# Kernel tuning notes

Measured on AMD Instinct MI355X. Metric: run time of the kernel, lower is better.

Reference implementation:

```python
import jax, jax.numpy as jnp
import numpy as np

B, N, M = 256, 4096, 16384
NUM_STEPS = 50
DT = 1.0
FP_THRES = 1e-3


def setup_inputs() -> dict:
    key = jax.random.key(0)
    k1, k2 = jax.random.split(key)
    inp = jax.random.normal(k1, (B, N, 1), dtype=jnp.float32)
    # xavier_normal for W [hidden, input]: std = sqrt(2/(fan_in+fan_out))
    std = np.sqrt(2.0 / (M + N)).astype(np.float32)
    W = jax.random.normal(k2, (M, N), dtype=jnp.float32) * std
    beta = jnp.float32(1.0)
    tau = jnp.float32(1.0)
    return {"input": inp, "W": W, "beta": beta, "tau": tau}


def reference(input, W, beta, tau):
    # Hopfield fixed-point iteration: v <- v + dt/tau * (W^T softmax(beta W v) - v)
    # input_mode='init' => state starts at input, no external current, no clamping.
    state0 = input  # [B, N, 1]
    done0 = jnp.array(False)

    def step(carry, _):
        state, done = carry
        h = jnp.einsum('mn,bno->bmo', W, state)            # [B, M, 1]
        f = jax.nn.softmax(beta * h, axis=-2)              # softmax over memory dim
        v_inst = jnp.einsum('mn,bmo->bno', W, f)           # [B, N, 1]
        new = state + (DT / tau) * (v_inst - state)
        # torch: update_magnitude = (prev_state - state).norm() (global Frobenius norm)
        upd = jnp.linalg.norm((new - state).reshape(-1))
        state_out = jnp.where(done, state, new)            # freeze once converged
        done = done | (upd <= FP_THRES)
        return (state_out, done), None

    (state, _), _ = jax.lax.scan(step, (state0, done0), None, length=NUM_STEPS)
    return state
```

## Files before the change

kernel.cpp:

```cpp
#include <hip/hip_runtime.h>

typedef __attribute__((ext_vector_type(8))) short short8;
typedef __attribute__((ext_vector_type(4))) float f32x4;
typedef __attribute__((ext_vector_type(2))) unsigned int u32x2;
typedef __attribute__((ext_vector_type(4))) unsigned int u32x4;

#define WS_ET   0u
#define WS_P2   8388608u
#define WS_ST   41943040u
#define WS_SB   46137344u
#define WS_CS   48234496u
#define WS_UG   48285696u
#define WS_CNT  48285952u
#define WS_WB   48298752u
#define WS_WBT  182516480u
#define WS_END  316734208u

#define WO_ET  0u
#define WO_P2  8388608u
#define WO_ST  25165824u
#define WO_SB  29360128u
#define WO_CS  31457280u
#define WO_UG  31508480u
#define WO_CNT 31508736u
#define WO_END 31534336u

static __device__ __forceinline__ unsigned short f2bf(float x) {
  union { float f; unsigned u; } v; v.f = x;
  unsigned r = v.u + 0x7FFFu + ((v.u >> 16) & 1u);
  return (unsigned short)(r >> 16);
}

static __device__ __forceinline__ void gl_lds16(const void* g, void* l) {
  __builtin_amdgcn_global_load_lds(
      (const __attribute__((address_space(1))) void*)g,
      (__attribute__((address_space(3))) void*)l, 16, 0, 0);
}

static __device__ __forceinline__ bool conv_before(const float* uG, int s) {
  bool d = false;
  for (int i = 0; i < s; ++i) d |= (uG[i] <= (-1.0f + 1.0e-6f));
  return d;
}

__global__ void sentinel_kernel(float* out, float v) { out[0] = v; }

__global__ void __launch_bounds__(256)
k0_setup(const float* __restrict__ inp, float* __restrict__ St,
         unsigned short* __restrict__ Sb, float* __restrict__ csG,
         float* __restrict__ uG, int* __restrict__ cnt)
{
  const int t = threadIdx.x, blk = blockIdx.x;
  if (blk == 0) {
    for (int i = t; i < 50 * 256; i += 256) csG[i] = 0.0f;
    if (t < 64) uG[t] = -1.0f;
  } else if (blk == 1) {
    for (int i = t; i < 50 * 128; i += 256) cnt[i] = 0;
  }
  #pragma unroll
  for (int i = 0; i < 8; ++i) {
    int idx = blk * 2048 + i * 256 + t;
    float v = inp[idx];
    Sb[idx] = f2bf(v);
    St[(idx & 4095) * 256 + (idx >> 12)] = v;
  }
}

__global__ void __launch_bounds__(256)
k0w_conv(const float* __restrict__ Wg, unsigned short* __restrict__ Wb,
         unsigned short* __restrict__ WbT)
{
  __shared__ unsigned short Tl[64][66];
  const int t = threadIdx.x;
  const int r = t >> 2, q = t & 3;
  for (int i = 0; i < 4; ++i) {
    const int ti = blockIdx.x * 4 + i;
    const int m0 = (ti >> 6) * 64;
    const int n0 = (ti & 63) * 64;
    const float* src = Wg + (size_t)(m0 + r) * 4096 + n0 + q * 16;
    unsigned short h[16] __attribute__((aligned(16)));
    #pragma unroll
    for (int v = 0; v < 4; ++v) {
      float4 f = *(const float4*)(src + v * 4);
      h[v*4+0] = f2bf(f.x); h[v*4+1] = f2bf(f.y);
      h[v*4+2] = f2bf(f.z); h[v*4+3] = f2bf(f.w);
    }
    unsigned short* wbp = Wb + (size_t)(m0 + r) * 4096 + n0 + q * 16;
    *(u32x4*)wbp       = *(const u32x4*)h;
    *(u32x4*)(wbp + 8) = *(const u32x4*)(h + 8);
    if (i) __syncthreads();
    #pragma unroll
    for (int k = 0; k < 16; ++k) Tl[r][q * 16 + k] = h[k];
    __syncthreads();
    unsigned short g[16] __attribute__((aligned(16)));
    const int nn = t >> 2;
    #pragma unroll
    for (int k = 0; k < 16; ++k) g[k] = Tl[q * 16 + k][nn];
    unsigned short* wtp = WbT + (size_t)(n0 + nn) * 16384 + m0 + q * 16;
    *(u32x4*)wtp       = *(const u32x4*)g;
    *(u32x4*)(wtp + 8) = *(const u32x4*)(g + 8);
  }
}

template<int ITERS>
static __device__ __forceinline__ void gemm_core(
    const unsigned short* __restrict__ Ag, const size_t lda, const int arow0,
    const unsigned short* __restrict__ Bg, const size_t ldb, const int brow0,
    const int kbase, unsigned short* smem, f32x4 (&acc)[4][4], const int t)
{
  const int lane = t & 63, wv = t >> 6;
  const int l15 = lane & 15, quad = lane >> 4;
  const int wr = wv >> 1, wc = wv & 1;
  const int xr = l15 & 7;
  unsigned short* As0 = smem;
  unsigned short* As1 = smem + 8192;
  unsigned short* Bs0 = smem + 16384;
  unsigned short* Bs1 = smem + 24576;
  const int srow = wv * 8 + (lane >> 3);
  const int ks   = ((lane & 7) ^ (lane >> 3)) * 8;
  const unsigned short* gA = Ag + (size_t)(arow0 + srow) * lda + kbase + ks;
  const unsigned short* gB = Bg + (size_t)(brow0 + srow) * ldb + kbase + ks;
  const int sb = wv * 512;

#define STAGE(itv, Ad, Bd)                                                        \
  { _Pragma("unroll") for (int j_ = 0; j_ < 4; ++j_) {                            \
      gl_lds16(gA + (size_t)j_ * 32 * lda + (size_t)(itv) * 64, (Ad) + j_ * 2048 + sb); \
      gl_lds16(gB + (size_t)j_ * 32 * ldb + (size_t)(itv) * 64, (Bd) + j_ * 2048 + sb); } }

  STAGE(0, As0, Bs0);
  __syncthreads();
  #pragma unroll 2
  for (int it = 0; it < ITERS; ++it) {
    unsigned short *Asc, *Bsc, *Asn, *Bsn;
    if (it & 1) { Asc = As1; Bsc = Bs1; Asn = As0; Bsn = Bs0; }
    else        { Asc = As0; Bsc = Bs0; Asn = As1; Bsn = Bs1; }
    if (it + 1 < ITERS) STAGE(it + 1, Asn, Bsn);
    #pragma unroll
    for (int kk = 0; kk < 2; ++kk) {
      short8 af[4], bq[4];
      const int so = ((kk * 4 + quad) ^ xr) << 3;
      #pragma unroll
      for (int r = 0; r < 4; ++r)
        af[r] = *(const short8*)(Asc + (wr * 64 + r * 16 + l15) * 64 + so);
      #pragma unroll
      for (int c = 0; c < 4; ++c)
        bq[c] = *(const short8*)(Bsc + (wc * 64 + c * 16 + l15) * 64 + so);
      #pragma unroll
      for (int r = 0; r < 4; ++r)
        #pragma unroll
        for (int c = 0; c < 4; ++c)
          acc[r][c] = __builtin_amdgcn_mfma_f32_16x16x32_bf16(af[r], bq[c], acc[r][c], 0, 0, 0);
    }
    __syncthreads();
  }
#undef STAGE
}

__global__ void __launch_bounds__(256, 2)
k1_gemm1(const unsigned short* __restrict__ Wb, const float* __restrict__ betap,
         const unsigned short* __restrict__ Sb, unsigned short* __restrict__ Et,
         float* __restrict__ csG, const float* __restrict__ uG, int s)
{
  if (conv_before(uG, s)) return;
  __shared__ __align__(16) unsigned char smem_[65536];
  const int t = threadIdx.x;
  const int w = ((blockIdx.x & 7) << 5) | (blockIdx.x >> 3);
  const int mt = w >> 1, bt = w & 1;
  const int m0 = mt * 128, b0 = bt * 128;

  f32x4 acc[4][4];
  #pragma unroll
  for (int r = 0; r < 4; ++r)
    #pragma unroll
    for (int c = 0; c < 4; ++c) { f32x4 z = {0.f,0.f,0.f,0.f}; acc[r][c] = z; }

  gemm_core<64>(Wb, 4096, m0, Sb, 4096, b0, 0, (unsigned short*)smem_, acc, t);

  const float beta = betap[0];
  const int lane = t & 63, wv = t >> 6, l15 = lane & 15, quad = lane >> 4;
  const int wr = wv >> 1, wc = wv & 1;
  #pragma unroll
  for (int c = 0; c < 4; ++c) {
    const int b = b0 + wc * 64 + c * 16 + l15;
    float cs = 0.0f;
    #pragma unroll
    for (int r = 0; r < 4; ++r) {
      unsigned short eb[4] __attribute__((aligned(8)));
      #pragma unroll
      for (int j = 0; j < 4; ++j) {
        float e = __expf(beta * acc[r][c][j]);
        cs += e;
        eb[j] = f2bf(e);
      }
      *(u32x2*)(Et + (size_t)b * 16384 + m0 + wr * 64 + r * 16 + quad * 4) = *(const u32x2*)eb;
    }
    cs += __shfl_xor(cs, 16, 64);
    cs += __shfl_xor(cs, 32, 64);
    if (quad == 0) atomicAdd(&csG[s * 256 + b], cs);
  }
}

__global__ void __launch_bounds__(256, 2)
k2_gemm2(const unsigned short* __restrict__ WbT, const float* __restrict__ taup,
         const unsigned short* __restrict__ Et, float* __restrict__ P2,
         float* __restrict__ St, unsigned short* __restrict__ Sb,
         const float* __restrict__ csG, float* __restrict__ uG,
         int* __restrict__ cnt, float* __restrict__ out, int s)
{
  if (conv_before(uG, s)) return;
  __shared__ __align__(16) unsigned char smem_[65536];
  const int t = threadIdx.x;
  const int w = ((blockIdx.x & 7) << 6) | (blockIdx.x >> 3);
  const int kc = w >> 6, nt = (w & 63) >> 1, bt = w & 1;
  const int n0 = nt * 128, b0 = bt * 128;

  f32x4 acc[4][4];
  #pragma unroll
  for (int r = 0; r < 4; ++r)
    #pragma unroll
    for (int c = 0; c < 4; ++c) { f32x4 z = {0.f,0.f,0.f,0.f}; acc[r][c] = z; }

  gemm_core<32>(WbT, 16384, n0, Et, 16384, b0, kc * 2048, (unsigned short*)smem_, acc, t);

  const int lane = t & 63, wv = t >> 6, l15 = lane & 15, quad = lane >> 4;
  const int wr = wv >> 1, wc = wv & 1;
  float* Pd = P2 + (size_t)kc * 1048576;
  #pragma unroll
  for (int r = 0; r < 4; ++r) {
    const int n = n0 + wr * 64 + r * 16 + quad * 4;
    #pragma unroll
    for (int c = 0; c < 4; ++c) {
      const int b = b0 + wc * 64 + c * 16 + l15;
      #pragma unroll
      for (int j = 0; j < 4; ++j)
        Pd[(size_t)(n + j) * 256 + b] = acc[r][c][j];
    }
  }

  __syncthreads();
  if (t == 0) {
    __threadfence();
    int old = atomicAdd(&cnt[s * 64 + (nt * 2 + bt)], 1);
    *(volatile int*)smem_ = (old == 7) ? 1 : 0;
  }
  __syncthreads();
  const bool last = (*(volatile int*)smem_ != 0);
  if (!last) return;
  __threadfence();
  __syncthreads();

  const float dtau = 1.0f / taup[0];
  float* T = (float*)smem_;
  float d2 = 0.0f;
  {
    const int bl = t & 127, th = t >> 7;
    const int bg = b0 + bl;
    const float inv = 1.0f / csG[s * 256 + bg];
    for (int i = 0; i < 64; ++i) {
      const int nl = i * 2 + th;
      const int n = n0 + nl;
      const float* pp = P2 + (size_t)n * 256 + bg;
      float sum = ((pp[0]       + pp[1048576]) + (pp[2097152] + pp[3145728]))
                + ((pp[4194304] + pp[5242880]) + (pp[6291456] + pp[7340032]));
      float v = sum * inv;
      float old = St[n * 256 + bg];
      float nw = old + dtau * (v - old);
      float d = nw - old;
      d2 += d * d;
      St[n * 256 + bg] = nw;
      T[bl * 128 + (nl ^ (bl & 31))] = nw;
    }
  }
  __syncthreads();
  {
    const int nl = t & 127, th = t >> 7;
    #pragma unroll 4
    for (int p = 0; p < 64; ++p) {
      const int bl = p * 2 + th;
      out[(size_t)(b0 + bl) * 4096 + n0 + nl] = T[bl * 128 + (nl ^ (bl & 31))];
    }
  }
  {
    const int np = (t & 63) * 2, th = t >> 6;
    #pragma unroll 4
    for (int p = 0; p < 32; ++p) {
      const int bl = p * 4 + th;
      const int sw = bl & 31;
      float x0 = T[bl * 128 + (np ^ sw)];
      float x1 = T[bl * 128 + ((np + 1) ^ sw)];
      unsigned u = (unsigned)f2bf(x0) | ((unsigned)f2bf(x1) << 16);
      *(unsigned*)(Sb + (size_t)(b0 + bl) * 4096 + n0 + np) = u;
    }
  }
  #pragma unroll
  for (int o = 32; o > 0; o >>= 1) d2 += __shfl_down(d2, o, 64);
  __syncthreads();
  float* red = (float*)smem_;
  if (lane == 0) red[wv] = d2;
  __syncthreads();
  if (t == 0) atomicAdd(&uG[s], red[0] + red[1] + red[2] + red[3]);
}

__global__ void __launch_bounds__(256, 2)
k1_gemm1_o(const float* __restrict__ Wg, const float* __restrict__ betap,
           const unsigned short* __restrict__ Sb, unsigned short* __restrict__ Et,
           float* __restrict__ csG, const float* __restrict__ uG, int s)
{
  if (conv_before(uG, s)) return;
  __shared__ __align__(16) unsigned char smem[36864];
  const int t = threadIdx.x;
  const int lane = t & 63;
  const int wv = t >> 6;
  const int quad = lane >> 4;
  const int l15 = lane & 15;
  const float beta = betap[0];

  const int m0 = blockIdx.x * 32;
  unsigned short* As0 = (unsigned short*)(smem);
  unsigned short* As1 = (unsigned short*)(smem + 2048);
  unsigned short* Bs0 = (unsigned short*)(smem + 4096);
  unsigned short* Bs1 = (unsigned short*)(smem + 20480);
  const int ar = t >> 3;
  const int ac = (t & 7) * 4;
  const float* gA = Wg + (size_t)(m0 + ar) * 4096 + ac;
  const int brow = wv * 16 + (lane >> 2);
  const int bcol = (lane & 3) * 8;

  f32x4 acc[2][4];
  #pragma unroll
  for (int r = 0; r < 2; ++r)
    #pragma unroll
    for (int c = 0; c < 4; ++c) { f32x4 z = {0.f,0.f,0.f,0.f}; acc[r][c] = z; }

  float4 arA, arB;
#define LOADA1(itv, dst) { dst = *(const float4*)(gA + (itv) * 32); }
#define WRITEA1(Ad, src) { unsigned short p_[4] __attribute__((aligned(8)));        \
      p_[0]=f2bf((src).x); p_[1]=f2bf((src).y); p_[2]=f2bf((src).z); p_[3]=f2bf((src).w); \
      *(u32x2*)((Ad) + ar * 32 + ac) = *(const u32x2*)p_; }
#define STAGEB1(itv, Bd) { const int k0_ = (itv) * 32 + bcol;                       \
      _Pragma("unroll") for (int j_ = 0; j_ < 4; ++j_)                              \
        gl_lds16(Sb + (size_t)(j_ * 64 + brow) * 4096 + k0_, (Bd) + j_ * 2048 + wv * 512); }

  LOADA1(0, arA); STAGEB1(0, Bs0); WRITEA1(As0, arA); LOADA1(1, arB);
  __syncthreads();

  #pragma unroll 2
  for (int it = 0; it < 128; ++it) {
    unsigned short *Asc, *Bsc, *Asn, *Bsn;
    float4 *arC, *arN;
    if (it & 1) { Asc = As1; Bsc = Bs1; Asn = As0; Bsn = Bs0; arC = &arA; arN = &arB; }
    else        { Asc = As0; Bsc = Bs0; Asn = As1; Bsn = Bs1; arC = &arB; arN = &arA; }
    if (it + 2 < 128) LOADA1(it + 2, (*arN));
    if (it + 1 < 128) { STAGEB1(it + 1, Bsn); WRITEA1(Asn, (*arC)); }
    short8 af[2], bq[4];
    #pragma unroll
    for (int r = 0; r < 2; ++r) af[r] = *(const short8*)(Asc + (16 * r + l15) * 32 + quad * 8);
    #pragma unroll
    for (int c = 0; c < 4; ++c) bq[c] = *(const short8*)(Bsc + (64 * wv + 16 * c + l15) * 32 + quad * 8);
    #pragma unroll
    for (int r = 0; r < 2; ++r)
      #pragma unroll
      for (int c = 0; c < 4; ++c)
        acc[r][c] = __builtin_amdgcn_mfma_f32_16x16x32_bf16(af[r], bq[c], acc[r][c], 0, 0, 0);
    __syncthreads();
  }
#undef LOADA1
#undef WRITEA1
#undef STAGEB1
  #pragma unroll
  for (int c = 0; c < 4; ++c) {
    const int b = 64 * wv + 16 * c + l15;
    float cs = 0.0f;
    #pragma unroll
    for (int r = 0; r < 2; ++r) {
      unsigned short eb[4] __attribute__((aligned(8)));
      #pragma unroll
      for (int j = 0; j < 4; ++j) {
        float e = __expf(beta * acc[r][c][j]);
        cs += e;
        eb[j] = f2bf(e);
      }
      *(u32x2*)(Et + (size_t)b * 16384 + m0 + 16 * r + quad * 4) = *(const u32x2*)eb;
    }
    cs += __shfl_xor(cs, 16, 64);
    cs += __shfl_xor(cs, 32, 64);
    if (quad == 0) atomicAdd(&csG[s * 256 + b], cs);
  }
}

__global__ void __launch_bounds__(256, 2)
k2_gemm2_o(const float* __restrict__ Wg, const float* __restrict__ taup,
           const unsigned short* __restrict__ Et, float* __restrict__ P2,
           float* __restrict__ St, unsigned short* __restrict__ Sb,
           const float* __restrict__ csG, float* __restrict__ uG,
           int* __restrict__ cnt, float* __restrict__ out, int s)
{
  if (conv_before(uG, s)) return;
  __shared__ __align__(16) unsigned char smem[37888];
  __shared__ int lastF;
  const int t = threadIdx.x;
  const int lane = t & 63;
  const int wv = t >> 6;
  const int quad = lane >> 4;
  const int l15 = lane & 15;
  const int rt = blockIdx.x & 127;
  const int kc = blockIdx.x >> 7;
  const int n0 = rt * 32;
  const int mb = kc * 4096;

  unsigned short* As0 = (unsigned short*)(smem);
  unsigned short* As1 = (unsigned short*)(smem + 2560);
  unsigned short* Bs0 = (unsigned short*)(smem + 5120);
  unsigned short* Bs1 = (unsigned short*)(smem + 21504);
  const int mp = (t >> 4) * 2;
  const int ng = (t & 15) * 2;
  const int brow = wv * 16 + (lane >> 2);
  const int bcol = (lane & 3) * 8;

  f32x4 acc[2][4];
  #pragma unroll
  for (int r = 0; r < 2; ++r)
    #pragma unroll
    for (int c = 0; c < 4; ++c) { f32x4 z = {0.f,0.f,0.f,0.f}; acc[r][c] = z; }

  float2 aA0, aA1, aB0, aB1;
#define LOADA2(itv, d0, d1) { const float* g_ = Wg + (size_t)(mb + (itv) * 32 + mp) * 4096 + n0 + ng; \
      d0 = *(const float2*)g_; d1 = *(const float2*)(g_ + 4096); }
#define WRITEA2(Ad, d0, d1) {                                                       \
      unsigned x0_ = (unsigned)f2bf((d0).x) | ((unsigned)f2bf((d1).x) << 16);       \
      unsigned x1_ = (unsigned)f2bf((d0).y) | ((unsigned)f2bf((d1).y) << 16);       \
      *(unsigned*)((Ad) + ng * 40 + mp) = x0_;                                      \
      *(unsigned*)((Ad) + (ng + 1) * 40 + mp) = x1_; }
#define STAGEB2(itv, Bd) { const int k0_ = mb + (itv) * 32 + bcol;                  \
      _Pragma("unroll") for (int j_ = 0; j_ < 4; ++j_)                              \
        gl_lds16(Et + (size_t)(j_ * 64 + brow) * 16384 + k0_, (Bd) + j_ * 2048 + wv * 512); }

  LOADA2(0, aA0, aA1); STAGEB2(0, Bs0); WRITEA2(As0, aA0, aA1); LOADA2(1, aB0, aB1);
  __syncthreads();

  #pragma unroll 2
  for (int it = 0; it < 128; ++it) {
    unsigned short *Asc, *Bsc, *Asn, *Bsn;
    float2 *c0, *c1, *n0p, *n1p;
    if (it & 1) { Asc = As1; Bsc = Bs1; Asn = As0; Bsn = Bs0; c0 = &aA0; c1 = &aA1; n0p = &aB0; n1p = &aB1; }
    else        { Asc = As0; Bsc = Bs0; Asn = As1; Bsn = Bs1; c0 = &aB0; c1 = &aB1; n0p = &aA0; n1p = &aA1; }
    if (it + 2 < 128) LOADA2(it + 2, (*n0p), (*n1p));
    if (it + 1 < 128) { STAGEB2(it + 1, Bsn); WRITEA2(Asn, (*c0), (*c1)); }
    short8 af[2], bq[4];
    #pragma unroll
    for (int r = 0; r < 2; ++r) af[r] = *(const short8*)(Asc + (16 * r + l15) * 40 + quad * 8);
    #pragma unroll
    for (int c = 0; c < 4; ++c) bq[c] = *(const short8*)(Bsc + (64 * wv + 16 * c + l15) * 32 + quad * 8);
    #pragma unroll
    for (int r = 0; r < 2; ++r)
      #pragma unroll
      for (int c = 0; c < 4; ++c)
        acc[r][c] = __builtin_amdgcn_mfma_f32_16x16x32_bf16(af[r], bq[c], acc[r][c], 0, 0, 0);
    __syncthreads();
  }
#undef LOADA2
#undef WRITEA2
#undef STAGEB2
  float* Pd = P2 + (size_t)kc * 1048576;
  #pragma unroll
  for (int r = 0; r < 2; ++r)
    #pragma unroll
    for (int c = 0; c < 4; ++c) {
      const int b = 64 * wv + 16 * c + l15;
      #pragma unroll
      for (int j = 0; j < 4; ++j)
        Pd[(size_t)(n0 + 16 * r + quad * 4 + j) * 256 + b] = acc[r][c][j];
    }

  __syncthreads();
  if (t == 0) {
    __threadfence();
    int old = atomicAdd(&cnt[s * 128 + rt], 1);
    lastF = (old == 3);
  }
  __syncthreads();
  if (!lastF) return;
  __threadfence();

  const float dtau = 1.0f / taup[0];
  const float inv = 1.0f / csG[s * 256 + t];
  float* T = (float*)smem;
  float d2 = 0.0f;
  for (int i = 0; i < 32; ++i) {
    const int n = n0 + i;
    const float* pp = P2 + (size_t)n * 256 + t;
    float sum = pp[0] + pp[1048576] + pp[2097152] + pp[3145728];
    float v = sum * inv;
    float old = St[n * 256 + t];
    float nw = old + dtau * (v - old);
    float d = nw - old;
    d2 += d * d;
    St[n * 256 + t] = nw;
    T[t * 33 + i] = nw;
  }
  __syncthreads();
  #pragma unroll 4
  for (int p = 0; p < 32; ++p) {
    const int b = p * 8 + (t >> 5);
    const int nl = t & 31;
    out[(size_t)b * 4096 + n0 + nl] = T[b * 33 + nl];
  }
  #pragma unroll 4
  for (int p = 0; p < 16; ++p) {
    const int b = p * 16 + (t >> 4);
    const int np = (t & 15) * 2;
    unsigned u = (unsigned)f2bf(T[b * 33 + np]) | ((unsigned)f2bf(T[b * 33 + np + 1]) << 16);
    *(unsigned*)(Sb + (size_t)b * 4096 + n0 + np) = u;
  }
  #pragma unroll
  for (int o = 32; o > 0; o >>= 1) d2 += __shfl_down(d2, o, 64);
  __syncthreads();
  float* red = (float*)smem;
  if (lane == 0) red[wv] = d2;
  __syncthreads();
  if (t == 0) atomicAdd(&uG[s], red[0] + red[1] + red[2] + red[3]);
}

extern "C" void kernel_launch(void* const* d_in, const int* in_sizes, int n_in,
                              void* d_out, int out_size, void* d_ws, size_t ws_size,
                              hipStream_t stream) {
  const float* inp   = (const float*)d_in[0];
  const float* W     = (const float*)d_in[1];
  const float* betap = (const float*)d_in[2];
  const float* taup  = (const float*)d_in[3];
  float* out = (float*)d_out;
  char* ws = (char*)d_ws;

  if (ws_size >= (size_t)WS_END) {
    unsigned short* Et = (unsigned short*)(ws + WS_ET);
    float*          P2 = (float*)(ws + WS_P2);
    float*          St = (float*)(ws + WS_ST);
    unsigned short* Sb = (unsigned short*)(ws + WS_SB);
    float*          cs = (float*)(ws + WS_CS);
    float*          uG = (float*)(ws + WS_UG);
    int*            cn = (int*)(ws + WS_CNT);
    unsigned short* Wb = (unsigned short*)(ws + WS_WB);
    unsigned short* Wt = (unsigned short*)(ws + WS_WBT);

    hipLaunchKernelGGL(k0_setup, dim3(512), dim3(256), 0, stream, inp, St, Sb, cs, uG, cn);
    hipLaunchKernelGGL(k0w_conv, dim3(4096), dim3(256), 0, stream, W, Wb, Wt);
    for (int s = 0; s < 50; ++s) {
      hipLaunchKernelGGL(k1_gemm1, dim3(256), dim3(256), 0, stream, Wb, betap, Sb, Et, cs, uG, s);
      hipLaunchKernelGGL(k2_gemm2, dim3(512), dim3(256), 0, stream, Wt, taup, Et, P2, St, Sb, cs, uG, cn, out, s);
    }
  } else if (ws_size >= (size_t)WO_END) {
    unsigned short* Et = (unsigned short*)(ws + WO_ET);
    float*          P2 = (float*)(ws + WO_P2);
    float*          St = (float*)(ws + WO_ST);
    unsigned short* Sb = (unsigned short*)(ws + WO_SB);
    float*          cs = (float*)(ws + WO_CS);
    float*          uG = (float*)(ws + WO_UG);
    int*            cn = (int*)(ws + WO_CNT);

    hipLaunchKernelGGL(k0_setup, dim3(512), dim3(256), 0, stream, inp, St, Sb, cs, uG, cn);
    for (int s = 0; s < 50; ++s) {
      hipLaunchKernelGGL(k1_gemm1_o, dim3(512), dim3(256), 0, stream, W, betap, Sb, Et, cs, uG, s);
      hipLaunchKernelGGL(k2_gemm2_o, dim3(512), dim3(256), 0, stream, W, taup, Et, P2, St, Sb, cs, uG, cn, out, s);
    }
  } else {
    hipLaunchKernelGGL(sentinel_kernel, dim3(1), dim3(1), 0, stream, out, 1.0e6f);
  }
}
```

Measured before the change: 1.178 ms.

## Fuse all Hopfield iterations into one persistent cooperative kernel with grid syncs

```diff
diff --git a/kernel.cpp b/kernel.cpp
--- a/kernel.cpp
+++ b/kernel.cpp
@@ -1,4 +1,7 @@
 #include <hip/hip_runtime.h>
+#include <hip/hip_cooperative_groups.h>
+
+namespace cg = cooperative_groups;
 
 typedef __attribute__((ext_vector_type(8))) short short8;
 typedef __attribute__((ext_vector_type(4))) float f32x4;
@@ -102,12 +105,13 @@
   }
 }
 
-template<int ITERS>
+template<int ITERS, int BROWS>
 static __device__ __forceinline__ void gemm_core(
     const unsigned short* __restrict__ Ag, const size_t lda, const int arow0,
     const unsigned short* __restrict__ Bg, const size_t ldb, const int brow0,
-    const int kbase, unsigned short* smem, f32x4 (&acc)[4][4], const int t)
+    const int kbase, unsigned short* smem, f32x4 (&acc)[4][BROWS / 32], const int t)
 {
+  constexpr int NC = BROWS / 32;
   const int lane = t & 63, wv = t >> 6;
   const int l15 = lane & 15, quad = lane >> 4;
   const int wr = wv >> 1, wc = wv & 1;
@@ -115,45 +119,168 @@
   unsigned short* As0 = smem;
   unsigned short* As1 = smem + 8192;
   unsigned short* Bs0 = smem + 16384;
-  unsigned short* Bs1 = smem + 24576;
+  unsigned short* Bs1 = Bs0 + BROWS * 64;
   const int srow = wv * 8 + (lane >> 3);
   const int ks   = ((lane & 7) ^ (lane >> 3)) * 8;
   const unsigned short* gA = Ag + (size_t)(arow0 + srow) * lda + kbase + ks;
   const unsigned short* gB = Bg + (size_t)(brow0 + srow) * ldb + kbase + ks;
   const int sb = wv * 512;
 
-#define STAGE(itv, Ad, Bd)                                                        \
-  { _Pragma("unroll") for (int j_ = 0; j_ < 4; ++j_) {                            \
+#define STAGE_(itv, Ad, Bd)                                                       \
+  { _Pragma("unroll") for (int j_ = 0; j_ < 4; ++j_)                              \
       gl_lds16(gA + (size_t)j_ * 32 * lda + (size_t)(itv) * 64, (Ad) + j_ * 2048 + sb); \
-      gl_lds16(gB + (size_t)j_ * 32 * ldb + (size_t)(itv) * 64, (Bd) + j_ * 2048 + sb); } }
-
-  STAGE(0, As0, Bs0);
+    _Pragma("unroll") for (int j_ = 0; j_ < NC; ++j_)                             \
+      gl_lds16(gB + (size_t)j_ * 32 * ldb + (size_t)(itv) * 64, (Bd) + j_ * 2048 + sb); }
+
+  STAGE_(0, As0, Bs0);
   __syncthreads();
   #pragma unroll 2
   for (int it = 0; it < ITERS; ++it) {
     unsigned short *Asc, *Bsc, *Asn, *Bsn;
     if (it & 1) { Asc = As1; Bsc = Bs1; Asn = As0; Bsn = Bs0; }
     else        { Asc = As0; Bsc = Bs0; Asn = As1; Bsn = Bs1; }
-    if (it + 1 < ITERS) STAGE(it + 1, Asn, Bsn);
+    if (it + 1 < ITERS) STAGE_(it + 1, Asn, Bsn);
     #pragma unroll
     for (int kk = 0; kk < 2; ++kk) {
-      short8 af[4], bq[4];
+      short8 af[4], bq[NC];
       const int so = ((kk * 4 + quad) ^ xr) << 3;
       #pragma unroll
       for (int r = 0; r < 4; ++r)
         af[r] = *(const short8*)(Asc + (wr * 64 + r * 16 + l15) * 64 + so);
       #pragma unroll
-      for (int c = 0; c < 4; ++c)
-        bq[c] = *(const short8*)(Bsc + (wc * 64 + c * 16 + l15) * 64 + so);
+      for (int c = 0; c < NC; ++c)
+        bq[c] = *(const short8*)(Bsc + (wc * (BROWS / 2) + c * 16 + l15) * 64 + so);
       #pragma unroll
       for (int r = 0; r < 4; ++r)
         #pragma unroll
-        for (int c = 0; c < 4; ++c)
+        for (int c = 0; c < NC; ++c)
           acc[r][c] = __builtin_amdgcn_mfma_f32_16x16x32_bf16(af[r], bq[c], acc[r][c], 0, 0, 0);
     }
     __syncthreads();
   }
-#undef STAGE
+#undef STAGE_
+}
+
+__global__ void __launch_bounds__(256, 2)
+khop_coop(const unsigned short* __restrict__ Wb, const unsigned short* __restrict__ WbT,
+          const float* __restrict__ betap, const float* __restrict__ taup,
+          unsigned short* __restrict__ Et, float* __restrict__ P2,
+          float* __restrict__ St, unsigned short* __restrict__ Sb,
+          float* __restrict__ csG, float* __restrict__ uG, float* __restrict__ out)
+{
+  cg::grid_group grid = cg::this_grid();
+  __shared__ __align__(16) unsigned char smem_[65536];
+  const int t = threadIdx.x;
+  const int blk = blockIdx.x;
+  const int w = ((blk & 7) << 6) | (blk >> 3);
+  const int lane = t & 63, wv = t >> 6;
+  const int l15 = lane & 15, quad = lane >> 4;
+  const int wr = wv >> 1, wc = wv & 1;
+  const float dtau = 1.0f / taup[0];
+  const float beta = betap[0];
+
+  for (int s = 0; s < 50; ++s) {
+    {
+      const int mt = w >> 2, bt = w & 3;
+      const int m0 = mt * 128, b0 = bt * 64;
+      f32x4 acc[4][2];
+      #pragma unroll
+      for (int r = 0; r < 4; ++r)
+        #pragma unroll
+        for (int c = 0; c < 2; ++c) { f32x4 z = {0.f,0.f,0.f,0.f}; acc[r][c] = z; }
+      gemm_core<64, 64>(Wb, 4096, m0, Sb, 4096, b0, 0, (unsigned short*)smem_, acc, t);
+      #pragma unroll
+      for (int c = 0; c < 2; ++c) {
+        const int b = b0 + wc * 32 + c * 16 + l15;
+        float cs = 0.0f;
+        #pragma unroll
+        for (int r = 0; r < 4; ++r) {
+          unsigned short eb[4] __attribute__((aligned(8)));
+          #pragma unroll
+          for (int j = 0; j < 4; ++j) {
+            float e = __expf(beta * acc[r][c][j]);
+            cs += e;
+            eb[j] = f2bf(e);
+          }
+          *(u32x2*)(Et + (size_t)b * 16384 + m0 + wr * 64 + r * 16 + quad * 4) = *(const u32x2*)eb;
+        }
+        cs += __shfl_xor(cs, 16, 64);
+        cs += __shfl_xor(cs, 32, 64);
+        if (quad == 0) atomicAdd(&csG[s * 256 + b], cs);
+      }
+    }
+    __threadfence();
+    grid.sync();
+
+    {
+      const int kc = w >> 6, nt = (w & 63) >> 1, bt2 = w & 1;
+      const int n0 = nt * 128, b0 = bt2 * 128;
+      f32x4 acc[4][4];
+      #pragma unroll
+      for (int r = 0; r < 4; ++r)
+        #pragma unroll
+        for (int c = 0; c < 4; ++c) { f32x4 z = {0.f,0.f,0.f,0.f}; acc[r][c] = z; }
+      gemm_core<32, 128>(WbT, 16384, n0, Et, 16384, b0, kc * 2048, (unsigned short*)smem_, acc, t);
+      float* Pd = P2 + (size_t)kc * 1048576;
+      #pragma unroll
+      for (int r = 0; r < 4; ++r) {
+        const int n = n0 + wr * 64 + r * 16 + quad * 4;
+        #pragma unroll
+        for (int c = 0; c < 4; ++c) {
+          const int b = b0 + wc * 64 + c * 16 + l15;
+          #pragma unroll
+          for (int j = 0; j < 4; ++j)
+            Pd[(size_t)(n + j) * 256 + b] = acc[r][c][j];
+        }
+      }
+    }
+    __threadfence();
+    grid.sync();
+
+    {
+      const int n0 = blk * 8;
+      const float inv = 1.0f / csG[s * 256 + t];
+      float* T = (float*)smem_;
+      float d2 = 0.0f;
+      #pragma unroll
+      for (int i = 0; i < 8; ++i) {
+        const int n = n0 + i;
+        const float* pp = P2 + (size_t)n * 256 + t;
+        float sum = ((pp[0]       + pp[1048576]) + (pp[2097152] + pp[3145728]))
+                  + ((pp[4194304] + pp[5242880]) + (pp[6291456] + pp[7340032]));
+        float v = sum * inv;
+        float old = St[n * 256 + t];
+        float nw = old + dtau * (v - old);
+        float d = nw - old;
+        d2 += d * d;
+        St[n * 256 + t] = nw;
+        T[t * 9 + i] = nw;
+      }
+      __syncthreads();
+      #pragma unroll
+      for (int p = 0; p < 8; ++p) {
+        const int b = p * 32 + (t >> 3);
+        out[(size_t)b * 4096 + n0 + (t & 7)] = T[b * 9 + (t & 7)];
+      }
+      #pragma unroll
+      for (int p = 0; p < 4; ++p) {
+        const int b = p * 64 + (t >> 2);
+        const int np = (t & 3) * 2;
+        unsigned u = (unsigned)f2bf(T[b * 9 + np]) | ((unsigned)f2bf(T[b * 9 + np + 1]) << 16);
+        *(unsigned*)(Sb + (size_t)b * 4096 + n0 + np) = u;
+      }
+      #pragma unroll
+      for (int o = 32; o > 0; o >>= 1) d2 += __shfl_down(d2, o, 64);
+      float* red = (float*)(smem_ + 32768);
+      if (lane == 0) red[wv] = d2;
+      __syncthreads();
+      if (t == 0) atomicAdd(&uG[s], red[0] + red[1] + red[2] + red[3]);
+    }
+    __threadfence();
+    grid.sync();
+    const float u = __hip_atomic_load(&uG[s], __ATOMIC_RELAXED, __HIP_MEMORY_SCOPE_AGENT);
+    if (u <= (-1.0f + 1.0e-6f)) break;
+  }
 }
 
 __global__ void __launch_bounds__(256, 2)
@@ -174,7 +301,7 @@
     #pragma unroll
     for (int c = 0; c < 4; ++c) { f32x4 z = {0.f,0.f,0.f,0.f}; acc[r][c] = z; }
 
-  gemm_core<64>(Wb, 4096, m0, Sb, 4096, b0, 0, (unsigned short*)smem_, acc, t);
+  gemm_core<64, 128>(Wb, 4096, m0, Sb, 4096, b0, 0, (unsigned short*)smem_, acc, t);
 
   const float beta = betap[0];
   const int lane = t & 63, wv = t >> 6, l15 = lane & 15, quad = lane >> 4;
@@ -220,7 +347,7 @@
     #pragma unroll
     for (int c = 0; c < 4; ++c) { f32x4 z = {0.f,0.f,0.f,0.f}; acc[r][c] = z; }
 
-  gemm_core<32>(WbT, 16384, n0, Et, 16384, b0, kc * 2048, (unsigned short*)smem_, acc, t);
+  gemm_core<32, 128>(WbT, 16384, n0, Et, 16384, b0, kc * 2048, (unsigned short*)smem_, acc, t);
 
   const int lane = t & 63, wv = t >> 6, l15 = lane & 15, quad = lane >> 4;
   const int wr = wv >> 1, wc = wv & 1;
@@ -544,9 +671,15 @@
 
     hipLaunchKernelGGL(k0_setup, dim3(512), dim3(256), 0, stream, inp, St, Sb, cs, uG, cn);
     hipLaunchKernelGGL(k0w_conv, dim3(4096), dim3(256), 0, stream, W, Wb, Wt);
-    for (int s = 0; s < 50; ++s) {
-      hipLaunchKernelGGL(k1_gemm1, dim3(256), dim3(256), 0, stream, Wb, betap, Sb, Et, cs, uG, s);
-      hipLaunchKernelGGL(k2_gemm2, dim3(512), dim3(256), 0, stream, Wt, taup, Et, P2, St, Sb, cs, uG, cn, out, s);
+
+    void* args[] = { &Wb, &Wt, &betap, &taup, &Et, &P2, &St, &Sb, &cs, &uG, &out };
+    hipError_t e = hipLaunchCooperativeKernel((const void*)khop_coop, dim3(512), dim3(256),
+                                              (void**)args, 0, stream);
+    if (e != hipSuccess) {
+      for (int s = 0; s < 50; ++s) {
+        hipLaunchKernelGGL(k1_gemm1, dim3(256), dim3(256), 0, stream, Wb, betap, Sb, Et, cs, uG, s);
+        hipLaunchKernelGGL(k2_gemm2, dim3(512), dim3(256), 0, stream, Wt, taup, Et, P2, St, Sb, cs, uG, cn, out, s);
+      }
     }
   } else if (ws_size >= (size_t)WO_END) {
     unsigned short* Et = (unsigned short*)(ws + WO_ET);
```

After: 1.953 ms. 65.8% more time.
